# Kernel tuning notes

Hardware: AMD Instinct MI355X
Metric: run time of the kernel (lower is better)

The kernel has to match this reference:

```python
import jax, jax.numpy as jnp
import numpy as np

NUM_HEADS = 4
HEAD_DIM = 128  # out_dim // num_heads = 512 // 4
TOP_K = 16
NEG_SLOPE = 0.2


def setup_inputs() -> dict:
    key = jax.random.key(0)
    k1, k2, k3, k4 = jax.random.split(key, 4)
    N, in_dim, out_dim = 4096, 1024, 512
    x = jax.random.normal(k1, (N, in_dim), dtype=jnp.float32)
    adj = jax.random.uniform(k2, (N, N), dtype=jnp.float32)  # all-positive, like softmax attn
    W = jax.random.normal(k3, (out_dim, in_dim), dtype=jnp.float32) * 0.02
    a = jax.random.normal(k4, (1, 2 * HEAD_DIM), dtype=jnp.float32) * 0.02
    return {"x": x, "adj": adj, "W": W, "a": a}


def reference(x, adj, W, a):
    N = x.shape[0]
    Wh = (x @ W.T).reshape(N, NUM_HEADS, HEAD_DIM)  # (N, H, D)

    # _sparsify_adj: keep top-k per row, binary mask
    k = min(TOP_K, N)
    _, topk_idx = jax.lax.top_k(adj, k)  # (N, k)
    rows = jnp.arange(N)[:, None]
    sparse = jnp.zeros_like(adj).at[rows, topk_idx].set(1.0)
    mask = sparse > 0  # (N_i, N_j)

    # a([Wh_i, Wh_j]) decomposed: a = [a_src | a_dst], score = s_i + s_j
    a_src, a_dst = a[0, :HEAD_DIM], a[0, HEAD_DIM:]
    s_i = jnp.einsum("nhd,d->nh", Wh, a_src)  # (N, H)
    s_j = jnp.einsum("nhd,d->nh", Wh, a_dst)  # (N, H)
    e = jax.nn.leaky_relu(s_i[:, None, :] + s_j[None, :, :], NEG_SLOPE)  # (N_i, N_j, H)
    e = jnp.where(mask[:, :, None], e, -jnp.inf)

    alpha = jax.nn.softmax(e, axis=1)  # softmax over neighbors j
    alpha = jnp.nan_to_num(alpha, nan=0.0)

    out = jnp.einsum("imh,mhd->ihd", alpha, Wh)  # weighted sum over j
    return jax.nn.elu(out.reshape(N, -1))  # (N, out_dim)
```

## Files before the change

### kernel.cpp

```cpp
#include <hip/hip_runtime.h>
#include <hip/hip_bf16.h>

#define N_NODES 4096
#define IN_DIM 1024
#define OUT_DIM 512
#define NUM_HEADS 4
#define HEAD_DIM 128
#define TOP_K 16
#define NEG_SLOPE 0.2f

typedef __attribute__((ext_vector_type(8))) short bf16x8;
typedef __attribute__((ext_vector_type(4))) float f32x4;

typedef __attribute__((address_space(3))) unsigned as3_u32;
typedef const __attribute__((address_space(1))) unsigned as1_u32;

static __device__ __forceinline__ void gld16(const void* g, void* l) {
    __builtin_amdgcn_global_load_lds((as1_u32*)g, (as3_u32*)l, 16, 0, 0);
}

__device__ __forceinline__ unsigned short f2bf(float f) {
    unsigned u = __float_as_uint(f);
    unsigned r = u + 0x7FFFu + ((u >> 16) & 1u);
    return (unsigned short)(r >> 16);
}
__device__ __forceinline__ float bf2f(unsigned short h) {
    return __uint_as_float(((unsigned)h) << 16);
}

__global__ __launch_bounds__(256) void prep_kernel(
    const float* __restrict__ src, unsigned short* __restrict__ dst)
{
    int t = blockIdx.x * 256 + threadIdx.x;
    int row = t >> 7, rem = t & 127, kb = rem >> 2, c = rem & 3;
    const float* s = src + (size_t)row * IN_DIM + kb * 32 + c * 8;
    float4 v0 = *(const float4*)s;
    float4 v1 = *(const float4*)(s + 4);
    float vv[8] = {v0.x, v0.y, v0.z, v0.w, v1.x, v1.y, v1.z, v1.w};
    bf16x8 H, L;
#pragma unroll
    for (int e = 0; e < 8; ++e) {
        unsigned short h = f2bf(vv[e]);
        H[e] = (short)h;
        L[e] = (short)f2bf(vv[e] - bf2f(h));
    }
    int sw = row & 7;
    unsigned short* base = dst + (size_t)row * 2048 + kb * 64;
    *(bf16x8*)(base + ((c ^ sw) << 3))       = H;
    *(bf16x8*)(base + (((c + 4) ^ sw) << 3)) = L;
}

#define GBM 128
#define GBN 64
#define NT  (IN_DIM / 32)

__global__ __launch_bounds__(512) void gemm_kernel(
    const unsigned short* __restrict__ xc, const unsigned short* __restrict__ wc,
    float* __restrict__ Wh)
{
    __shared__ __align__(16) unsigned short As[2][GBM * 64];
    __shared__ __align__(16) unsigned short Bs[2][GBN * 64];

    const int tid  = threadIdx.x;
    const int bm   = blockIdx.x, bn = blockIdx.y;
    const int wave = tid >> 6,   lane = tid & 63;
    const int wm   = wave >> 2,  wn = wave & 3;
    const int lr   = lane & 15,  lk = lane >> 4;

    f32x4 acc[4];
#pragma unroll
    for (int i = 0; i < 4; ++i) acc[i] = (f32x4){0.f, 0.f, 0.f, 0.f};

    auto stage = [&](int buf, int kt) {
#pragma unroll
        for (int seg = 0; seg < 2; ++seg) {
            int ci = seg * 512 + tid;
            int row = ci >> 3, p = ci & 7;
            const char* src = (const char*)xc +
                ((size_t)(bm * GBM + row) * 4096 + (size_t)kt * 128 + p * 16);
            gld16(src, (char*)&As[buf][0] + (size_t)ci * 16);
        }
        {
            int ci = tid;
            int row = ci >> 3, p = ci & 7;
            const char* src = (const char*)wc +
                ((size_t)(bn * GBN + row) * 4096 + (size_t)kt * 128 + p * 16);
            gld16(src, (char*)&Bs[buf][0] + (size_t)ci * 16);
        }
    };

    stage(0, 0);
    __syncthreads();
    int cur = 0;
    for (int kt = 0; kt < NT; ++kt) {
        if (kt + 1 < NT) stage(cur ^ 1, kt + 1);

        bf16x8 bh, bl;
        {
            int rb = wn * 16 + lr, sw = (rb & 7) << 3;
            bh = *(const bf16x8*)&Bs[cur][rb * 64 + ((lk * 8) ^ sw)];
            bl = *(const bf16x8*)&Bs[cur][rb * 64 + ((32 + lk * 8) ^ sw)];
        }
#pragma unroll
        for (int mi = 0; mi < 4; ++mi) {
            int r = wm * 64 + mi * 16 + lr, sw = (r & 7) << 3;
            bf16x8 ah = *(const bf16x8*)&As[cur][r * 64 + ((lk * 8) ^ sw)];
            bf16x8 al = *(const bf16x8*)&As[cur][r * 64 + ((32 + lk * 8) ^ sw)];
            acc[mi] = __builtin_amdgcn_mfma_f32_16x16x32_bf16(ah, bh, acc[mi], 0, 0, 0);
            acc[mi] = __builtin_amdgcn_mfma_f32_16x16x32_bf16(ah, bl, acc[mi], 0, 0, 0);
            acc[mi] = __builtin_amdgcn_mfma_f32_16x16x32_bf16(al, bh, acc[mi], 0, 0, 0);
        }
        __syncthreads();
        cur ^= 1;
    }

#pragma unroll
    for (int mi = 0; mi < 4; ++mi)
#pragma unroll
        for (int r = 0; r < 4; ++r) {
            int row_g = bm * GBM + wm * 64 + mi * 16 + lk * 4 + r;
            int col_g = bn * GBN + wn * 16 + lr;
            Wh[(size_t)row_g * OUT_DIM + col_g] = acc[mi][r];
        }
}

__global__ __launch_bounds__(256) void score_kernel(
    const float* __restrict__ Wh, const float* __restrict__ a,
    float* __restrict__ s_src, float* __restrict__ s_dst)
{
    const int n = blockIdx.x;
    const int h = threadIdx.x >> 6, lane = threadIdx.x & 63;
    const float* whp = Wh + (size_t)n * OUT_DIM + h * HEAD_DIM;
    float ss = 0.f, sd = 0.f;
#pragma unroll
    for (int i = 0; i < 2; ++i) {
        int d = lane + i * 64;
        float w = whp[d];
        ss += w * a[d];
        sd += w * a[HEAD_DIM + d];
    }
#pragma unroll
    for (int m = 1; m < 64; m <<= 1) {
        ss += __shfl_xor(ss, m);
        sd += __shfl_xor(sd, m);
    }
    if (lane == 0) {
        s_src[n * NUM_HEADS + h] = ss;
        s_dst[n * NUM_HEADS + h] = sd;
    }
}

#define TK_THRESH 0.988f
#define TK_CAP 128

__global__ __launch_bounds__(256) void topk_kernel(
    const float* __restrict__ adj, int* __restrict__ topk)
{
    const int wave = threadIdx.x >> 6, lane = threadIdx.x & 63;
    const int row  = blockIdx.x * 4 + wave;
    const float* rp = adj + (size_t)row * N_NODES;
    __shared__ unsigned long long cand[4][TK_CAP];

    float v[64];
#pragma unroll
    for (int i = 0; i < 16; ++i) {
        float4 q = *(const float4*)(rp + i * 256 + lane * 4);
        v[i * 4 + 0] = q.x; v[i * 4 + 1] = q.y; v[i * 4 + 2] = q.z; v[i * 4 + 3] = q.w;
    }
    int* op = topk + (size_t)row * TOP_K;

    const unsigned long long lmask = (1ull << lane) - 1ull;
    int cnt = 0;
#pragma unroll
    for (int s = 0; s < 64; ++s) {
        int g = (s >> 2) * 256 + lane * 4 + (s & 3);
        bool p = v[s] >= TK_THRESH;
        unsigned long long m = __ballot(p);
        if (p) {
            int pos = cnt + __popcll(m & lmask);
            if (pos < TK_CAP) {
                unsigned b  = __float_as_uint(v[s]);
                unsigned mo = b ^ (unsigned)(((int)b >> 31) | 0x80000000);
                cand[wave][pos] =
                    ((unsigned long long)mo << 32) | (unsigned)(N_NODES - 1 - g);
            }
        }
        cnt += __popcll(m);
    }

    if (cnt >= TOP_K && cnt <= TK_CAP) {
        for (int j = cnt + lane; j < TK_CAP; j += 64) cand[wave][j] = 0ull;
        unsigned long long c0 = cand[wave][lane], c1 = cand[wave][lane + 64];
        for (int r = 0; r < TOP_K; ++r) {
            unsigned long long b = c0 > c1 ? c0 : c1;
#pragma unroll
            for (int m = 1; m < 64; m <<= 1) {
                unsigned long long o = __shfl_xor(b, m);
                b = o > b ? o : b;
            }
            if (lane == 0) op[r] = N_NODES - 1 - (int)(unsigned)(b & 0xFFFFFFFFu);
            if (c0 == b) c0 = 0ull;
            if (c1 == b) c1 = 0ull;
        }
    } else {
        for (int r = 0; r < TOP_K; ++r) {
            float bv = -INFINITY; int bg = 0x7fffffff;
#pragma unroll
            for (int s = 0; s < 64; ++s) {
                int g = (s >> 2) * 256 + lane * 4 + (s & 3);
                bool better = (v[s] > bv) || (v[s] == bv && g < bg);
                bv = better ? v[s] : bv;
                bg = better ? g : bg;
            }
#pragma unroll
            for (int m = 1; m < 64; m <<= 1) {
                float ov = __shfl_xor(bv, m);
                int   og = __shfl_xor(bg, m);
                bool better = (ov > bv) || (ov == bv && og < bg);
                bv = better ? ov : bv;
                bg = better ? og : bg;
            }
            if (lane == 0) op[r] = bg;
#pragma unroll
            for (int s = 0; s < 64; ++s) {
                int g = (s >> 2) * 256 + lane * 4 + (s & 3);
                if (g == bg) v[s] = -INFINITY;
            }
        }
    }
}

__global__ __launch_bounds__(256) void aggregate_kernel(
    const float* __restrict__ Wh, const int* __restrict__ topk,
    const float* __restrict__ s_src, const float* __restrict__ s_dst,
    float* __restrict__ out)
{
    const int i = blockIdx.x, t = threadIdx.x;
    __shared__ int   sidx[TOP_K];
    __shared__ float salpha[TOP_K][NUM_HEADS];
    __shared__ float ssrc[NUM_HEADS];

    if (t < TOP_K) sidx[t] = topk[(size_t)i * TOP_K + t];
    if (t < NUM_HEADS) ssrc[t] = s_src[i * NUM_HEADS + t];
    __syncthreads();

    if (t < TOP_K * NUM_HEADS) {
        int m = t >> 2, h = t & 3;
        float e = ssrc[h] + s_dst[sidx[m] * NUM_HEADS + h];
        e = (e >= 0.f) ? e : NEG_SLOPE * e;
        salpha[m][h] = e;
    }
    __syncthreads();

    if (t < NUM_HEADS) {
        int h = t;
        float mx = -INFINITY;
#pragma unroll
        for (int m = 0; m < TOP_K; ++m) mx = fmaxf(mx, salpha[m][h]);
        float ex[TOP_K]; float sum = 0.f;
#pragma unroll
        for (int m = 0; m < TOP_K; ++m) { ex[m] = expf(salpha[m][h] - mx); sum += ex[m]; }
        float inv = 1.f / sum;
#pragma unroll
        for (int m = 0; m < TOP_K; ++m) salpha[m][h] = ex[m] * inv;
    }
    __syncthreads();

#pragma unroll
    for (int rep = 0; rep < 2; ++rep) {
        int c = rep * 256 + t;
        int h = c >> 7;
        float acc = 0.f;
#pragma unroll
        for (int m = 0; m < TOP_K; ++m)
            acc += salpha[m][h] * Wh[(size_t)sidx[m] * OUT_DIM + c];
        out[(size_t)i * OUT_DIM + c] = (acc > 0.f) ? acc : (expf(acc) - 1.f);
    }
}

extern "C" void kernel_launch(void* const* d_in, const int* in_sizes, int n_in,
                              void* d_out, int out_size, void* d_ws, size_t ws_size,
                              hipStream_t stream) {
    const float* x   = (const float*)d_in[0];
    const float* adj = (const float*)d_in[1];
    const float* W   = (const float*)d_in[2];
    const float* a   = (const float*)d_in[3];
    float* out = (float*)d_out;

    char* ws = (char*)d_ws;
    float*          Wh    = (float*)ws;
    unsigned short* xc    = (unsigned short*)(ws + (8u << 20));
    unsigned short* wc    = (unsigned short*)(ws + (24u << 20));
    float*          s_src = (float*)(ws + (26u << 20));
    float*          s_dst = s_src + N_NODES * NUM_HEADS;
    int*            topkb = (int*)(s_dst + N_NODES * NUM_HEADS);

    prep_kernel<<<(N_NODES * 128) / 256, 256, 0, stream>>>(x, xc);
    prep_kernel<<<(OUT_DIM * 128) / 256, 256, 0, stream>>>(W, wc);
    gemm_kernel<<<dim3(N_NODES / GBM, OUT_DIM / GBN), 512, 0, stream>>>(xc, wc, Wh);
    score_kernel<<<N_NODES, 256, 0, stream>>>(Wh, a, s_src, s_dst);
    topk_kernel<<<N_NODES / 4, 256, 0, stream>>>(adj, topkb);
    aggregate_kernel<<<N_NODES, 256, 0, stream>>>(Wh, topkb, s_src, s_dst, out);
}
```

Baseline: 174.1 us.

## Fuse score computation into GEMM epilogue and merge prep launches

Merges the two prep conversions and zeroing of the score buffers into one launch. Shrinks the GEMM tile to 64x64 with 256 threads and an XCD-aware block remap. Computes the per-head attention scores in the GEMM epilogue through shuffle reductions and atomics, which removes the separate score kernel. Rewrites the aggregate softmax as a wave-level shuffle reduction to cut the extra barriers. The cost is atomic contention and nondeterministic summation order for the scores, plus smaller GEMM tiles that reuse less data.

```diff
diff --git a/kernel.cpp b/kernel.cpp
--- a/kernel.cpp
+++ b/kernel.cpp
@@ -28,10 +28,9 @@
     return __uint_as_float(((unsigned)h) << 16);
 }
 
-__global__ __launch_bounds__(256) void prep_kernel(
-    const float* __restrict__ src, unsigned short* __restrict__ dst)
-{
-    int t = blockIdx.x * 256 + threadIdx.x;
+__device__ __forceinline__ void conv_row(const float* __restrict__ src,
+                                         unsigned short* __restrict__ dst, int t)
+{
     int row = t >> 7, rem = t & 127, kb = rem >> 2, c = rem & 3;
     const float* s = src + (size_t)row * IN_DIM + kb * 32 + c * 8;
     float4 v0 = *(const float4*)s;
@@ -50,22 +49,41 @@
     *(bf16x8*)(base + (((c + 4) ^ sw) << 3)) = L;
 }
 
-#define GBM 128
+__global__ __launch_bounds__(256) void prep_kernel(
+    const float* __restrict__ x, const float* __restrict__ W,
+    unsigned short* __restrict__ xc, unsigned short* __restrict__ wc,
+    float* __restrict__ szero)
+{
+    int b = blockIdx.x, tid = threadIdx.x;
+    if (b < 2048) {
+        conv_row(x, xc, b * 256 + tid);
+    } else if (b < 2304) {
+        conv_row(W, wc, (b - 2048) * 256 + tid);
+    } else {
+        int t = (b - 2304) * 256 + tid;
+        ((float4*)szero)[t] = (float4){0.f, 0.f, 0.f, 0.f};
+    }
+}
+
+#define GBM 64
 #define GBN 64
 #define NT  (IN_DIM / 32)
 
-__global__ __launch_bounds__(512) void gemm_kernel(
+__global__ __launch_bounds__(256) void gemm_kernel(
     const unsigned short* __restrict__ xc, const unsigned short* __restrict__ wc,
-    float* __restrict__ Wh)
+    const float* __restrict__ a, float* __restrict__ Wh,
+    float* __restrict__ s_src, float* __restrict__ s_dst)
 {
     __shared__ __align__(16) unsigned short As[2][GBM * 64];
     __shared__ __align__(16) unsigned short Bs[2][GBN * 64];
 
-    const int tid  = threadIdx.x;
-    const int bm   = blockIdx.x, bn = blockIdx.y;
-    const int wave = tid >> 6,   lane = tid & 63;
-    const int wm   = wave >> 2,  wn = wave & 3;
-    const int lr   = lane & 15,  lk = lane >> 4;
+    const int tid = threadIdx.x;
+    const int id  = blockIdx.x;
+    const int xcd = id & 7, seq = id >> 3;
+    const int bm  = xcd * 8 + (seq >> 3), bn = seq & 7;
+
+    const int wn = tid >> 6, lane = tid & 63;
+    const int lr = lane & 15, lk = lane >> 4;
 
     f32x4 acc[4];
 #pragma unroll
@@ -74,18 +92,13 @@
     auto stage = [&](int buf, int kt) {
 #pragma unroll
         for (int seg = 0; seg < 2; ++seg) {
-            int ci = seg * 512 + tid;
+            int ci = seg * 256 + tid;
             int row = ci >> 3, p = ci & 7;
-            const char* src = (const char*)xc +
-                ((size_t)(bm * GBM + row) * 4096 + (size_t)kt * 128 + p * 16);
-            gld16(src, (char*)&As[buf][0] + (size_t)ci * 16);
-        }
-        {
-            int ci = tid;
-            int row = ci >> 3, p = ci & 7;
-            const char* src = (const char*)wc +
-                ((size_t)(bn * GBN + row) * 4096 + (size_t)kt * 128 + p * 16);
-            gld16(src, (char*)&Bs[buf][0] + (size_t)ci * 16);
+            size_t off = (size_t)kt * 128 + p * 16;
+            gld16((const char*)xc + ((size_t)(bm * GBM + row) * 4096 + off),
+                  (char*)&As[buf][0] + (size_t)ci * 16);
+            gld16((const char*)wc + ((size_t)(bn * GBN + row) * 4096 + off),
+                  (char*)&Bs[buf][0] + (size_t)ci * 16);
         }
     };
 
@@ -103,7 +116,7 @@
         }
 #pragma unroll
         for (int mi = 0; mi < 4; ++mi) {
-            int r = wm * 64 + mi * 16 + lr, sw = (r & 7) << 3;
+            int r = mi * 16 + lr, sw = (r & 7) << 3;
             bf16x8 ah = *(const bf16x8*)&As[cur][r * 64 + ((lk * 8) ^ sw)];
             bf16x8 al = *(const bf16x8*)&As[cur][r * 64 + ((32 + lk * 8) ^ sw)];
             acc[mi] = __builtin_amdgcn_mfma_f32_16x16x32_bf16(ah, bh, acc[mi], 0, 0, 0);
@@ -114,39 +127,35 @@
         cur ^= 1;
     }
 
-#pragma unroll
-    for (int mi = 0; mi < 4; ++mi)
+    const int col_g = bn * GBN + wn * 16 + lr;
+    const int h = col_g >> 7, d = col_g & (HEAD_DIM - 1);
+    const float ca = a[d], cb = a[HEAD_DIM + d];
+#pragma unroll
+    for (int mi = 0; mi < 4; ++mi) {
+        float ss[4], sd[4];
 #pragma unroll
         for (int r = 0; r < 4; ++r) {
-            int row_g = bm * GBM + wm * 64 + mi * 16 + lk * 4 + r;
-            int col_g = bn * GBN + wn * 16 + lr;
-            Wh[(size_t)row_g * OUT_DIM + col_g] = acc[mi][r];
-        }
-}
-
-__global__ __launch_bounds__(256) void score_kernel(
-    const float* __restrict__ Wh, const float* __restrict__ a,
-    float* __restrict__ s_src, float* __restrict__ s_dst)
-{
-    const int n = blockIdx.x;
-    const int h = threadIdx.x >> 6, lane = threadIdx.x & 63;
-    const float* whp = Wh + (size_t)n * OUT_DIM + h * HEAD_DIM;
-    float ss = 0.f, sd = 0.f;
-#pragma unroll
-    for (int i = 0; i < 2; ++i) {
-        int d = lane + i * 64;
-        float w = whp[d];
-        ss += w * a[d];
-        sd += w * a[HEAD_DIM + d];
-    }
-#pragma unroll
-    for (int m = 1; m < 64; m <<= 1) {
-        ss += __shfl_xor(ss, m);
-        sd += __shfl_xor(sd, m);
-    }
-    if (lane == 0) {
-        s_src[n * NUM_HEADS + h] = ss;
-        s_dst[n * NUM_HEADS + h] = sd;
+            int row_g = bm * GBM + mi * 16 + lk * 4 + r;
+            float v = acc[mi][r];
+            Wh[(size_t)row_g * OUT_DIM + col_g] = v;
+            ss[r] = v * ca;
+            sd[r] = v * cb;
+        }
+#pragma unroll
+        for (int s = 1; s < 16; s <<= 1)
+#pragma unroll
+            for (int r = 0; r < 4; ++r) {
+                ss[r] += __shfl_xor(ss[r], s);
+                sd[r] += __shfl_xor(sd[r], s);
+            }
+        if (lr == 0) {
+#pragma unroll
+            for (int r = 0; r < 4; ++r) {
+                int row_g = bm * GBM + mi * 16 + lk * 4 + r;
+                atomicAdd(&s_src[row_g * NUM_HEADS + h], ss[r]);
+                atomicAdd(&s_dst[row_g * NUM_HEADS + h], sd[r]);
+            }
+        }
     }
 }
 
@@ -238,31 +247,22 @@
     const int i = blockIdx.x, t = threadIdx.x;
     __shared__ int   sidx[TOP_K];
     __shared__ float salpha[TOP_K][NUM_HEADS];
-    __shared__ float ssrc[NUM_HEADS];
-
-    if (t < TOP_K) sidx[t] = topk[(size_t)i * TOP_K + t];
-    if (t < NUM_HEADS) ssrc[t] = s_src[i * NUM_HEADS + t];
-    __syncthreads();
-
-    if (t < TOP_K * NUM_HEADS) {
+
+    if (t < 64) {
+        int idxv = 0;
+        if (t < TOP_K) { idxv = topk[(size_t)i * TOP_K + t]; sidx[t] = idxv; }
         int m = t >> 2, h = t & 3;
-        float e = ssrc[h] + s_dst[sidx[m] * NUM_HEADS + h];
+        int im = __shfl(idxv, m);
+        float e = s_src[i * NUM_HEADS + h] + s_dst[im * NUM_HEADS + h];
         e = (e >= 0.f) ? e : NEG_SLOPE * e;
-        salpha[m][h] = e;
-    }
-    __syncthreads();
-
-    if (t < NUM_HEADS) {
-        int h = t;
-        float mx = -INFINITY;
-#pragma unroll
-        for (int m = 0; m < TOP_K; ++m) mx = fmaxf(mx, salpha[m][h]);
-        float ex[TOP_K]; float sum = 0.f;
-#pragma unroll
-        for (int m = 0; m < TOP_K; ++m) { ex[m] = expf(salpha[m][h] - mx); sum += ex[m]; }
-        float inv = 1.f / sum;
-#pragma unroll
-        for (int m = 0; m < TOP_K; ++m) salpha[m][h] = ex[m] * inv;
+        float mx = e;
+#pragma unroll
+        for (int s = 4; s < 64; s <<= 1) mx = fmaxf(mx, __shfl_xor(mx, s));
+        float ex = expf(e - mx);
+        float sum = ex;
+#pragma unroll
+        for (int s = 4; s < 64; s <<= 1) sum += __shfl_xor(sum, s);
+        salpha[m][h] = ex / sum;
     }
     __syncthreads();
 
@@ -295,10 +295,8 @@
     float*          s_dst = s_src + N_NODES * NUM_HEADS;
     int*            topkb = (int*)(s_dst + N_NODES * NUM_HEADS);
 
-    prep_kernel<<<(N_NODES * 128) / 256, 256, 0, stream>>>(x, xc);
-    prep_kernel<<<(OUT_DIM * 128) / 256, 256, 0, stream>>>(W, wc);
-    gemm_kernel<<<dim3(N_NODES / GBM, OUT_DIM / GBN), 512, 0, stream>>>(xc, wc, Wh);
-    score_kernel<<<N_NODES, 256, 0, stream>>>(Wh, a, s_src, s_dst);
+    prep_kernel<<<2336, 256, 0, stream>>>(x, W, xc, wc, s_src);
+    gemm_kernel<<<512, 256, 0, stream>>>(xc, wc, a, Wh, s_src, s_dst);
     topk_kernel<<<N_NODES / 4, 256, 0, stream>>>(adj, topkb);
     aggregate_kernel<<<N_NODES, 256, 0, stream>>>(Wh, topkb, s_src, s_dst, out);
 }
```

Result: slower. 181.2 us (+4.1%).
